# Kernel tuning notes

Measured on AMD Instinct MI355X. Metric: run time of the kernel, lower is better.

Reference implementation:

```python
import math
import jax, jax.numpy as jnp
import numpy as np

N = 2048          # batch size
D = 256           # embedding_dim
MEM = 16384       # memory_size
ANOMALY_WEIGHT = 1.0
TEMP = 0.1
MOMENTUM = 0.01
NCLS = 2          # binary phishing labels -> max(labels.max()+1, 2) == 2


def setup_inputs() -> dict:
    key = jax.random.key(0)
    ks = jax.random.split(key, 10)
    s = 1.0 / math.sqrt(D)  # nn.Linear default init range
    return {
        'z': jax.random.normal(ks[0], (N, D), jnp.float32),
        'labels': jax.random.randint(ks[1], (N,), 0, NCLS),
        'memory': jax.random.normal(ks[2], (MEM, D), jnp.float32),
        'memory_weights': jax.random.uniform(ks[3], (MEM,), jnp.float32),
        'running_mean': jnp.zeros((D,), jnp.float32),
        'running_cov': jnp.eye(D, dtype=jnp.float32),
        'Wq': jax.random.uniform(ks[4], (D, D), jnp.float32, -s, s),
        'bq': jax.random.uniform(ks[5], (D,), jnp.float32, -s, s),
        'Wk': jax.random.uniform(ks[6], (D, D), jnp.float32, -s, s),
        'bk': jax.random.uniform(ks[7], (D,), jnp.float32, -s, s),
        'Wv': jax.random.uniform(ks[8], (D, D), jnp.float32, -s, s),
        'bv': jax.random.uniform(ks[9], (D,), jnp.float32, -s, s),
    }


def reference(z, labels, memory, memory_weights, running_mean, running_cov,
              Wq, bq, Wk, bk, Wv, bv):
    # ---- update(z.detach(), labels): entire update path is detached in torch ----
    z_sg = jax.lax.stop_gradient(z)

    # _update_stats: EMA of batch mean / covariance (done before importance)
    mu = z_sg.mean(axis=0)                                  # [D]
    zc = z_sg - mu
    cov = zc.T @ zc / max(N - 1, 1)                         # [D, D]
    rm = (1.0 - MOMENTUM) * running_mean + MOMENTUM * mu
    rc = (1.0 - MOMENTUM) * running_cov + MOMENTUM * cov

    # _mahalanobis with updated running stats
    c = z_sg - rm
    cov_inv = jnp.linalg.inv(rc + 1e-6 * jnp.eye(D, dtype=rc.dtype))
    dist = jnp.sqrt(jnp.clip(jnp.einsum('nd,de,ne->n', c, cov_inv, c), 1e-8))
    a_norm = (dist - dist.min()) / (dist.max() - dist.min() + 1e-8)

    # _mi_proxy: KL(batch label dist || uniform), broadcast to all items
    counts = jnp.zeros((NCLS,), z.dtype).at[labels].add(1.0)
    p = counts / jnp.clip(counts.sum(), 1.0)
    # p / uniform == p * NCLS; clip inside log for safety (both classes present)
    kl = jnp.clip((p * jnp.log(jnp.clip(p * NCLS, 1e-8))).sum(), 0.0)
    importance = (1.0 + ANOMALY_WEIGHT * a_norm) * kl       # [N]

    # serial top-1 priority-queue eviction, in descending-importance order
    order = jnp.argsort(-importance)
    z_ord = z_sg[order]
    imp_ord = importance[order]

    def evict_step(state, inp):
        mem, w = state
        zi, imp = inp
        j = jnp.argmin(w)                   # weakest memory slot
        rep = imp > w[j]
        mem = mem.at[j].set(jnp.where(rep, zi, mem[j]))
        w = w.at[j].set(jnp.where(rep, imp, w[j]))
        return (mem, w), None

    (mem, _), _ = jax.lax.scan(evict_step, (memory, memory_weights), (z_ord, imp_ord))

    # ---- query(z): cross-attention over the (full) updated memory ----
    Q = z @ Wq.T + bq                       # [N, D]
    K = mem @ Wk.T + bk                     # [MEM, D]
    V = mem @ Wv.T + bv                     # [MEM, D]
    sc = (Q @ K.T) / math.sqrt(D)           # [N, MEM]
    attn = jax.nn.softmax(sc / TEMP, axis=-1)
    return z + 0.5 * (attn @ V)
```

## Files before the change

kernel.cpp:

```cpp
#include <hip/hip_runtime.h>
#include <math.h>

#define NB   2048
#define DE   256
#define MEMN 16384
#define CAND_CAP 256
#define FSPL 16
#define FKPS 1024
#define FIT  32

typedef __attribute__((ext_vector_type(8)))  short  short8;
typedef __attribute__((ext_vector_type(16))) float  float16;
typedef __attribute__((ext_vector_type(4)))  unsigned uint4v;
typedef __attribute__((ext_vector_type(2)))  unsigned uint2v;

static const size_t OFF_QB   = 0;
static const size_t OFF_KB   = 262144;
static const size_t OFF_VTB  = 2359296;
static const size_t OFF_LP   = 4456448;
static const size_t OFF_OPB  = 4521984;
static const size_t SO_A    = 0;
static const size_t SO_X    = 65536;
static const size_t SO_MUP  = 131072;
static const size_t SO_DIST = 147456;

__device__ inline unsigned short f2bf(float f) {
  unsigned u = __float_as_uint(f);
  unsigned r = (u + 0x7fffu + ((u >> 16) & 1u)) >> 16;
  return (unsigned short)r;
}
__device__ inline float bf2f(unsigned short s) {
  return __uint_as_float((unsigned)s << 16);
}

__device__ inline unsigned cvtpk_bf16(float lo, float hi) {
  unsigned r;
  asm("v_cvt_pk_bf16_f32 %0, %1, %2" : "=v"(r) : "v"(lo), "v"(hi));
  return r;
}

__device__ inline void halfswap(unsigned& lo, unsigned& hi, int h) {
#if __has_builtin(__builtin_amdgcn_permlane32_swap)
  (void)h;
  uint2v r = __builtin_amdgcn_permlane32_swap(lo, hi, false, false);
  lo = r.x; hi = r.y;
#else
  unsigned a = (unsigned)__shfl_xor((int)lo, 32, 64);
  unsigned b = (unsigned)__shfl_xor((int)hi, 32, 64);
  unsigned nlo = (h == 0) ? lo : b;
  unsigned nhi = (h == 0) ? a  : hi;
  lo = nlo; hi = nhi;
#endif
}

__device__ inline void bitonic_sort_u64(unsigned long long* key, int n, int tid, int nth) {
  for (int k = 2; k <= n; k <<= 1) {
    for (int j = k >> 1; j > 0; j >>= 1) {
      __syncthreads();
      for (int i = tid; i < n; i += nth) {
        int ixj = i ^ j;
        if (ixj > i) {
          unsigned long long a = key[i], b = key[ixj];
          bool up = ((i & k) == 0);
          if ((a > b) == up) { key[i] = b; key[ixj] = a; }
        }
      }
    }
  }
  __syncthreads();
}

__global__ __launch_bounds__(256) void mupart_kernel(const float* __restrict__ z,
                                                     float* __restrict__ mup,
                                                     float* __restrict__ Az) {
  int d = threadIdx.x;
  int r0 = blockIdx.x * 32;
  float4 zero4 = {0.f, 0.f, 0.f, 0.f};
  *(float4*)&Az[(size_t)blockIdx.x * 1024 + threadIdx.x * 4] = zero4;
  float s = 0.f;
  for (int r = 0; r < 32; ++r) s += z[(size_t)(r0 + r) * DE + d];
  mup[blockIdx.x * DE + d] = s;
}

__global__ __launch_bounds__(256) void covpart_kernel(const float* __restrict__ z,
                                                      float* __restrict__ A) {
  __shared__ float As[16][68];
  __shared__ float Bs[16][68];
  int tid = threadIdx.x, tx = tid & 15, ty = tid >> 4;
  int i0 = blockIdx.x * 64, j0 = blockIdx.y * 64;
  int nbase = blockIdx.z * 128;
  float acc[4][4] = {};
  for (int nt = 0; nt < 8; ++nt) {
    int n0 = nbase + nt * 16;
    for (int e = tid; e < 1024; e += 256) {
      int c = e & 63, nn = e >> 6;
      As[nn][c] = z[(size_t)(n0 + nn) * DE + i0 + c];
      Bs[nn][c] = z[(size_t)(n0 + nn) * DE + j0 + c];
    }
    __syncthreads();
#pragma unroll
    for (int nn = 0; nn < 16; ++nn) {
      float4 a4 = *(const float4*)&As[nn][ty * 4];
      float4 b4 = *(const float4*)&Bs[nn][tx * 4];
      acc[0][0] += a4.x*b4.x; acc[0][1] += a4.x*b4.y; acc[0][2] += a4.x*b4.z; acc[0][3] += a4.x*b4.w;
      acc[1][0] += a4.y*b4.x; acc[1][1] += a4.y*b4.y; acc[1][2] += a4.y*b4.z; acc[1][3] += a4.y*b4.w;
      acc[2][0] += a4.z*b4.x; acc[2][1] += a4.z*b4.y; acc[2][2] += a4.z*b4.z; acc[2][3] += a4.z*b4.w;
      acc[3][0] += a4.w*b4.x; acc[3][1] += a4.w*b4.y; acc[3][2] += a4.w*b4.z; acc[3][3] += a4.w*b4.w;
    }
    __syncthreads();
  }
  for (int r = 0; r < 4; ++r) {
    int i = i0 + ty * 4 + r;
    for (int c = 0; c < 4; ++c) {
      int j = j0 + tx * 4 + c;
      atomicAdd(&A[(size_t)i * DE + j], acc[r][c]);
    }
  }
}

__global__ __launch_bounds__(256) void gemmx_kernel(const float* __restrict__ ZtZ,
                                                    const float* __restrict__ rcov,
                                                    const float* __restrict__ mup,
                                                    float* __restrict__ X) {
  __shared__ float Ea[16][17];
  __shared__ float Eb[16][17];
  __shared__ float mus[256];
  int t = threadIdx.x, tx = t & 15, ty = t >> 4;
  int i0 = blockIdx.x * 16, j0 = blockIdx.y * 16;
  {
    float s = 0.f;
    for (int b = 0; b < 64; ++b) s += mup[b * DE + t];
    mus[t] = s;
  }
  __syncthreads();
  const float c1 = 0.01f / (float)(NB - 1);
  const float invN = 1.0f / (float)NB;
  float acc = 0.f;
  for (int k0 = 0; k0 < 256; k0 += 16) {
    int c = k0 + tx;
    {
      int r = i0 + ty;
      float base = 0.99f * rcov[(size_t)r * DE + c] +
                   c1 * (ZtZ[(size_t)r * DE + c] - mus[r] * mus[c] * invN);
      float e = -base;
      if (r == c) e += 1.0f - 1e-6f;
      Ea[ty][tx] = e;
    }
    {
      int r = j0 + ty;
      float base = 0.99f * rcov[(size_t)r * DE + c] +
                   c1 * (ZtZ[(size_t)r * DE + c] - mus[r] * mus[c] * invN);
      float e = -base;
      if (r == c) e += 1.0f - 1e-6f;
      Eb[ty][tx] = e;
    }
    __syncthreads();
#pragma unroll
    for (int k = 0; k < 16; ++k) acc += Ea[ty][k] * Eb[tx][k];
    __syncthreads();
  }
  int r = i0 + ty, c = j0 + tx;
  float base = 0.99f * rcov[(size_t)r * DE + c] +
               c1 * (ZtZ[(size_t)r * DE + c] - mus[r] * mus[c] * invN);
  float e = -base;
  if (r == c) e += 1.0f - 1e-6f;
  X[(size_t)r * DE + c] = acc + e + ((r == c) ? 1.0f : 0.0f);
}

__global__ __launch_bounds__(256) void dist_kernel(const float* __restrict__ z,
                                                   const float* __restrict__ rmean,
                                                   const float* __restrict__ mup,
                                                   const float* __restrict__ X,
                                                   float* __restrict__ dist) {
  __shared__ float cc[4][256];
  __shared__ float4 red[256];
  int n0 = blockIdx.x * 4, i = threadIdx.x;
  float s = 0.f;
  for (int b = 0; b < 64; ++b) s += mup[b * DE + i];
  float rmi = 0.99f * rmean[i] + 0.01f * s * (1.0f / (float)NB);
#pragma unroll
  for (int r = 0; r < 4; ++r) cc[r][i] = z[(size_t)(n0 + r) * DE + i] - rmi;
  __syncthreads();
  float y0 = 0.f, y1 = 0.f, y2 = 0.f, y3 = 0.f;
#pragma unroll 8
  for (int j = 0; j < DE; ++j) {
    float x = X[(size_t)j * DE + i];
    y0 += x * cc[0][j]; y1 += x * cc[1][j]; y2 += x * cc[2][j]; y3 += x * cc[3][j];
  }
  float4 v;
  v.x = y0 * cc[0][i]; v.y = y1 * cc[1][i]; v.z = y2 * cc[2][i]; v.w = y3 * cc[3][i];
  red[i] = v;
  __syncthreads();
  for (int sH = 128; sH > 0; sH >>= 1) {
    if (i < sH) {
      float4 a = red[i], b = red[i + sH];
      a.x += b.x; a.y += b.y; a.z += b.z; a.w += b.w;
      red[i] = a;
    }
    __syncthreads();
  }
  if (i < 4) {
    float4 tt = red[0];
    float d = (i == 0) ? tt.x : (i == 1) ? tt.y : (i == 2) ? tt.z : tt.w;
    dist[n0 + i] = sqrtf(fmaxf(d, 1e-8f));
  }
}

__global__ __launch_bounds__(1024) void update_kernel(const float* __restrict__ dist,
                                                      const int* __restrict__ labels,
                                                      const float* __restrict__ weights,
                                                      const float* __restrict__ z,
                                                      float* __restrict__ memory) {
  __shared__ unsigned long long ikeys[NB];
  __shared__ unsigned long long ck[CAND_CAP];
  __shared__ unsigned long long mred[1024];
  __shared__ int slots[CAND_CAP], srcs[CAND_CAP];
  __shared__ float smin[1024], smax[1024];
  __shared__ int scnt[1024];
  __shared__ float s_kl, s_dmin, s_inv;
  __shared__ int s_ccnt, s_m, s_stop;
  int t = threadIdx.x;

  float mn = 1e30f, mx = -1e30f; int c1 = 0;
  for (int n = t; n < NB; n += 1024) {
    float d = dist[n];
    mn = fminf(mn, d); mx = fmaxf(mx, d);
    c1 += labels[n];
  }
  smin[t] = mn; smax[t] = mx; scnt[t] = c1;
  __syncthreads();
  for (int s = 512; s > 0; s >>= 1) {
    if (t < s) {
      smin[t] = fminf(smin[t], smin[t + s]);
      smax[t] = fmaxf(smax[t], smax[t + s]);
      scnt[t] += scnt[t + s];
    }
    __syncthreads();
  }
  if (t == 0) {
    float p1 = (float)scnt[0] / (float)NB;
    float p0 = (float)(NB - scnt[0]) / (float)NB;
    float kl = p0 * logf(fmaxf(2.f * p0, 1e-8f)) + p1 * logf(fmaxf(2.f * p1, 1e-8f));
    s_kl = fmaxf(kl, 0.f);
    s_dmin = smin[0];
    s_inv = 1.0f / (smax[0] - smin[0] + 1e-8f);
    s_ccnt = 0; s_m = 0; s_stop = 0;
  }
  __syncthreads();
  float kl = s_kl;

  for (int n = t; n < NB; n += 1024) {
    float imp = (1.0f + (dist[n] - s_dmin) * s_inv) * kl;
    ikeys[n] = ((unsigned long long)(unsigned)(~__float_as_uint(imp)) << 32) | (unsigned)n;
  }
  float thresh = 2.f * kl;
  for (int j = t; j < MEMN; j += 1024) {
    float wv = weights[j];
    if (wv < thresh) {
      int p = atomicAdd(&s_ccnt, 1);
      if (p < CAND_CAP) ck[p] = ((unsigned long long)__float_as_uint(wv) << 32) | (unsigned)j;
    }
  }
  __syncthreads();
  int C = s_ccnt; if (C > CAND_CAP) C = CAND_CAP;
  for (int i = t; i < CAND_CAP; i += 1024)
    if (i >= C) ck[i] = 0xFFFFFFFFFFFFFFFFULL;
  bitonic_sort_u64(ck, CAND_CAP, t, 1024);

  float prevv = 0.f;
  for (int i = 0; i < C; ++i) {
    unsigned long long mymin = ikeys[t] < ikeys[t + 1024] ? ikeys[t] : ikeys[t + 1024];
    mred[t] = mymin;
    __syncthreads();
    for (int s = 512; s > 0; s >>= 1) {
      if (t < s) { if (mred[t + s] < mred[t]) mred[t] = mred[t + s]; }
      __syncthreads();
    }
    if (t == 0) {
      unsigned long long best = mred[0];
      float im = __uint_as_float(~(unsigned)(best >> 32));
      float wv = __uint_as_float((unsigned)(ck[i] >> 32));
      bool ok = (im > wv) && (i == 0 || prevv >= wv);
      if (ok) {
        slots[s_m] = (int)(ck[i] & 0xffffffffULL);
        srcs[s_m]  = (int)(best & 0xffffffffULL);
        s_m++;
        prevv = im;
        ikeys[(int)(best & 0xffffffffULL)] = ~0ULL;
      } else {
        s_stop = 1;
      }
    }
    __syncthreads();
    if (s_stop) break;
  }
  int m = s_m;
  for (int e = t; e < m * DE; e += 1024) {
    int i = e >> 8, d = e & 255;
    memory[(size_t)slots[i] * DE + d] = z[(size_t)srcs[i] * DE + d];
  }
}

__global__ __launch_bounds__(256, 1) void qkv_kernel(
    const float* __restrict__ z, const float* __restrict__ memory,
    const float* __restrict__ Wq, const float* __restrict__ bq,
    const float* __restrict__ Wk, const float* __restrict__ bk,
    const float* __restrict__ Wv, const float* __restrict__ bv,
    unsigned short* __restrict__ Qbf, unsigned short* __restrict__ Kbf,
    unsigned short* __restrict__ Vtb) {
  __shared__ unsigned short Bsh[64 * 264];
  int flat = blockIdx.x;
  const float *Af, *Bf, *bias;
  unsigned short* C;
  int bias_row, vtile, gx, gy, ldC;
  if (flat < 64) {
    gx = flat & 15; gy = flat >> 4;
    Af = z; Bf = Wq; bias = bq; bias_row = 0; vtile = 0; C = Qbf; ldC = DE;
  } else if (flat < 576) {
    int f = flat - 64; gx = f & 127; gy = f >> 7;
    Af = memory; Bf = Wk; bias = bk; bias_row = 0; vtile = 0; C = Kbf; ldC = DE;
  } else {
    int f = flat - 576; gx = f & 1; gy = f >> 1;
    Af = Wv; Bf = memory; bias = bv; bias_row = 1; vtile = 1; C = Vtb; ldC = 0;
  }

  int tid = threadIdx.x;
  int w = tid >> 6, lane = tid & 63;
  int m = lane & 31, h = lane >> 5;
  int arow = gx * 128 + w * 32 + m;
  int n0 = gy * 64;

  short8 af[16];
#pragma unroll
  for (int kc = 0; kc < 16; ++kc) {
    const float* src = &Af[(size_t)arow * DE + kc * 16 + h * 8];
    float4 f0 = *(const float4*)&src[0];
    float4 f1 = *(const float4*)&src[4];
    short8 v;
    v[0] = (short)f2bf(f0.x); v[1] = (short)f2bf(f0.y);
    v[2] = (short)f2bf(f0.z); v[3] = (short)f2bf(f0.w);
    v[4] = (short)f2bf(f1.x); v[5] = (short)f2bf(f1.y);
    v[6] = (short)f2bf(f1.z); v[7] = (short)f2bf(f1.w);
    af[kc] = v;
  }
  {
    int r = tid >> 2, q = tid & 3;
    const float* src = &Bf[(size_t)(n0 + r) * DE + q * 64];
    unsigned short* dst = &Bsh[r * 264 + q * 64];
#pragma unroll
    for (int j = 0; j < 8; ++j) {
      float4 f0 = *(const float4*)&src[j * 8];
      float4 f1 = *(const float4*)&src[j * 8 + 4];
      short8 v;
      v[0] = (short)f2bf(f0.x); v[1] = (short)f2bf(f0.y);
      v[2] = (short)f2bf(f0.z); v[3] = (short)f2bf(f0.w);
      v[4] = (short)f2bf(f1.x); v[5] = (short)f2bf(f1.y);
      v[6] = (short)f2bf(f1.z); v[7] = (short)f2bf(f1.w);
      *(short8*)&dst[j * 8] = v;
    }
  }
  __syncthreads();

  float16 a0 = {}, a1 = {};
#pragma unroll
  for (int kc = 0; kc < 16; ++kc) {
    short8 b0 = *(const short8*)&Bsh[(0 * 32 + m) * 264 + kc * 16 + h * 8];
    short8 b1 = *(const short8*)&Bsh[(1 * 32 + m) * 264 + kc * 16 + h * 8];
    a0 = __builtin_amdgcn_mfma_f32_32x32x16_bf16(af[kc], b0, a0, 0, 0, 0);
    a1 = __builtin_amdgcn_mfma_f32_32x32x16_bf16(af[kc], b1, a1, 0, 0, 0);
  }
#pragma unroll
  for (int r = 0; r < 16; ++r) {
    int rr = (r & 3) + 8 * (r >> 2) + 4 * h;
    int orow = gx * 128 + w * 32 + rr;
    int oc0 = n0 + m, oc1 = n0 + 32 + m;
    float bb0 = bias_row ? bias[orow] : bias[oc0];
    float bb1 = bias_row ? bias[orow] : bias[oc1];
    if (!vtile) {
      C[(size_t)orow * ldC + oc0] = f2bf(a0[r] + bb0);
      C[(size_t)orow * ldC + oc1] = f2bf(a1[r] + bb1);
    } else {
      C[(size_t)(oc0 >> 5) * 8192 + (size_t)orow * 32 + (oc0 & 31)] = f2bf(a0[r] + bb0);
      C[(size_t)(oc1 >> 5) * 8192 + (size_t)orow * 32 + (oc1 & 31)] = f2bf(a1[r] + bb1);
    }
  }
}

__global__ __launch_bounds__(256, 2) void flash_kernel(
    const unsigned short* __restrict__ Qb, const unsigned short* __restrict__ Kb,
    const unsigned short* __restrict__ Vtb, unsigned short* __restrict__ Opb,
    float* __restrict__ Lp) {
  __shared__ unsigned short Ks[32 * 264];
  __shared__ unsigned short Vs[128 * 40];

  int tid = threadIdx.x;
  int w = tid >> 6, lane = tid & 63;
  int m = lane & 31, h = lane >> 5;
  int sp = blockIdx.x, qg = blockIdx.y, dh = blockIdx.z;
  int myrow = qg * 128 + w * 32 + m;

  short8 qf[16];
#pragma unroll
  for (int kc = 0; kc < 16; ++kc)
    qf[kc] = *(const short8*)&Qb[(size_t)myrow * DE + kc * 16 + h * 8];

  float16 O[4] = {};
  float lacc = 0.f;

  short8 kreg[4], vreg[2];
  {
    int kb = sp * FKPS;
#pragma unroll
    for (int i = 0; i < 4; ++i) {
      int c = i * 256 + tid, kr = c >> 5, kc = c & 31;
      kreg[i] = *(const short8*)&Kb[(size_t)(kb + kr) * DE + kc * 8];
    }
    const unsigned short* vg = &Vtb[(size_t)(kb >> 5) * 8192 + (size_t)dh * 4096];
#pragma unroll
    for (int i = 0; i < 2; ++i) {
      int c = i * 256 + tid;
      vreg[i] = *(const short8*)&vg[c * 8];
    }
  }

  for (int it = 0; it < FIT; ++it) {
    __syncthreads();
#pragma unroll
    for (int i = 0; i < 4; ++i) {
      int c = i * 256 + tid, kr = c >> 5, kc = c & 31;
      *(short8*)&Ks[kr * 264 + kc * 8] = kreg[i];
    }
#pragma unroll
    for (int i = 0; i < 2; ++i) {
      int c = i * 256 + tid, dr = c >> 2, dc = c & 3;
      *(short8*)&Vs[dr * 40 + dc * 8] = vreg[i];
    }
    if (it + 1 < FIT) {
      int kb = sp * FKPS + (it + 1) * 32;
#pragma unroll
      for (int i = 0; i < 4; ++i) {
        int c = i * 256 + tid, kr = c >> 5, kc = c & 31;
        kreg[i] = *(const short8*)&Kb[(size_t)(kb + kr) * DE + kc * 8];
      }
      const unsigned short* vg = &Vtb[(size_t)(kb >> 5) * 8192 + (size_t)dh * 4096];
#pragma unroll
      for (int i = 0; i < 2; ++i) {
        int c = i * 256 + tid;
        vreg[i] = *(const short8*)&vg[c * 8];
      }
    }
    __syncthreads();

    float16 s0 = {}, s1 = {};
    __builtin_amdgcn_s_setprio(1);
#pragma unroll
    for (int kc = 0; kc < 16; kc += 2) {
      short8 b0 = *(const short8*)&Ks[m * 264 + kc * 16 + h * 8];
      short8 b1 = *(const short8*)&Ks[m * 264 + (kc + 1) * 16 + h * 8];
      s0 = __builtin_amdgcn_mfma_f32_32x32x16_bf16(b0, qf[kc], s0, 0, 0, 0);
      s1 = __builtin_amdgcn_mfma_f32_32x32x16_bf16(b1, qf[kc + 1], s1, 0, 0, 0);
    }
    __builtin_amdgcn_s_setprio(0);

    float p[16];
#pragma unroll
    for (int r = 0; r < 16; ++r)
      p[r] = exp2f(fmaf(s0[r] + s1[r], 0.90168440f, -16.0f));

    lacc += ((p[0] + p[1]) + (p[2] + p[3])) + ((p[4] + p[5]) + (p[6] + p[7])) +
            ((p[8] + p[9]) + (p[10] + p[11])) + ((p[12] + p[13]) + (p[14] + p[15]));

    unsigned c0 = cvtpk_bf16(p[0],  p[1]);
    unsigned c1 = cvtpk_bf16(p[2],  p[3]);
    unsigned c2 = cvtpk_bf16(p[4],  p[5]);
    unsigned c3 = cvtpk_bf16(p[6],  p[7]);
    unsigned c4 = cvtpk_bf16(p[8],  p[9]);
    unsigned c5 = cvtpk_bf16(p[10], p[11]);
    unsigned c6 = cvtpk_bf16(p[12], p[13]);
    unsigned c7 = cvtpk_bf16(p[14], p[15]);
    halfswap(c0, c2, h);
    halfswap(c1, c3, h);
    halfswap(c4, c6, h);
    halfswap(c5, c7, h);
    uint4v w0v = {c0, c1, c2, c3};
    uint4v w1v = {c4, c5, c6, c7};
    short8 pa0 = __builtin_bit_cast(short8, w0v);
    short8 pa1 = __builtin_bit_cast(short8, w1v);

    __builtin_amdgcn_s_setprio(1);
#pragma unroll
    for (int ct = 0; ct < 4; ++ct) {
      short8 vb0 = *(const short8*)&Vs[(ct * 32 + m) * 40 + h * 8];
      short8 vb1 = *(const short8*)&Vs[(ct * 32 + m) * 40 + 16 + h * 8];
      O[ct] = __builtin_amdgcn_mfma_f32_32x32x16_bf16(pa0, vb0, O[ct], 0, 0, 0);
      O[ct] = __builtin_amdgcn_mfma_f32_32x32x16_bf16(pa1, vb1, O[ct], 0, 0, 0);
    }
    __builtin_amdgcn_s_setprio(0);
  }

  size_t ob = ((size_t)sp * NB + qg * 128 + w * 32) * DE + dh * 128;
#pragma unroll
  for (int ct = 0; ct < 4; ++ct)
#pragma unroll
    for (int r = 0; r < 16; ++r) {
      int rr = (r & 3) + 8 * (r >> 2) + 4 * h;
      Opb[ob + (size_t)rr * DE + ct * 32 + m] = f2bf(O[ct][r]);
    }
  float ltot = lacc + __shfl_xor(lacc, 32, 64);
  if (dh == 0 && h == 0)
    Lp[sp * NB + qg * 128 + w * 32 + m] = ltot;
}

__global__ __launch_bounds__(256) void combine_kernel(const float* __restrict__ z,
                                                      const unsigned short* __restrict__ Opb,
                                                      const float* __restrict__ Lp,
                                                      float* __restrict__ out) {
  int n = blockIdx.x, c = threadIdx.x;
  float num = 0.f, den = 0.f;
#pragma unroll
  for (int s = 0; s < FSPL; ++s) {
    den += Lp[s * NB + n];
    num += bf2f(Opb[((size_t)s * NB + n) * DE + c]);
  }
  size_t base = (size_t)n * DE + c;
  out[base] = z[base] + 0.5f * num / den;
}

extern "C" void kernel_launch(void* const* d_in, const int* in_sizes, int n_in,
                              void* d_out, int out_size, void* d_ws, size_t ws_size,
                              hipStream_t stream) {
  (void)in_sizes; (void)n_in; (void)out_size; (void)ws_size;
  const float* z       = (const float*)d_in[0];
  const int*   labels  = (const int*)d_in[1];
  float*       memory  = (float*)d_in[2];
  const float* weights = (const float*)d_in[3];
  const float* rmean   = (const float*)d_in[4];
  const float* rcov    = (const float*)d_in[5];
  const float* Wq      = (const float*)d_in[6];
  const float* bq      = (const float*)d_in[7];
  const float* Wk      = (const float*)d_in[8];
  const float* bk      = (const float*)d_in[9];
  const float* Wv      = (const float*)d_in[10];
  const float* bv      = (const float*)d_in[11];
  float* out = (float*)d_out;
  float* ws  = (float*)d_ws;

  unsigned short* Qbf = (unsigned short*)(ws + OFF_QB);
  unsigned short* Kbf = (unsigned short*)(ws + OFF_KB);
  unsigned short* Vtb = (unsigned short*)(ws + OFF_VTB);
  float* Lp           = ws + OFF_LP;
  unsigned short* Opb = (unsigned short*)(ws + OFF_OPB);
  float* SB    = ws + OFF_OPB;
  float* A     = SB + SO_A;
  float* X     = SB + SO_X;
  float* mup   = SB + SO_MUP;
  float* dist  = SB + SO_DIST;

  mupart_kernel<<<64, 256, 0, stream>>>(z, mup, A);
  covpart_kernel<<<dim3(4, 4, 16), 256, 0, stream>>>(z, A);
  gemmx_kernel<<<dim3(16, 16), 256, 0, stream>>>(A, rcov, mup, X);
  dist_kernel<<<NB / 4, 256, 0, stream>>>(z, rmean, mup, X, dist);
  update_kernel<<<1, 1024, 0, stream>>>(dist, labels, weights, z, memory);
  qkv_kernel<<<1088, 256, 0, stream>>>(z, memory, Wq, bq, Wk, bk, Wv, bv, Qbf, Kbf, Vtb);
  flash_kernel<<<dim3(FSPL, NB / 128, 2), 256, 0, stream>>>(Qbf, Kbf, Vtb, Opb, Lp);
  combine_kernel<<<NB, 256, 0, stream>>>(z, Opb, Lp, out);
}
```

Baseline: 260.0 us.

## Use warp-shuffle reductions in update kernel and double flash key tile size

The update kernel's block-wide shared-memory tree reductions become wave-level shuffle reductions. The serial eviction loop now keeps per-wave minima and recomputes only the wave whose entry was consumed, which removes about ten barriers per eviction step. The flash kernel processes 64 keys per iteration instead of 32, halving the number of barrier-separated load/store stages. The cost is doubled LDS and register use for K/V staging, which may lower occupancy.

```diff
diff --git a/kernel.cpp b/kernel.cpp
--- a/kernel.cpp
+++ b/kernel.cpp
@@ -7,7 +7,7 @@
 #define CAND_CAP 256
 #define FSPL 16
 #define FKPS 1024
-#define FIT  32
+#define FIT  16
 
 typedef __attribute__((ext_vector_type(8)))  short  short8;
 typedef __attribute__((ext_vector_type(16))) float  float16;
@@ -213,13 +213,14 @@
                                                       float* __restrict__ memory) {
   __shared__ unsigned long long ikeys[NB];
   __shared__ unsigned long long ck[CAND_CAP];
-  __shared__ unsigned long long mred[1024];
+  __shared__ unsigned long long gmin[16];
   __shared__ int slots[CAND_CAP], srcs[CAND_CAP];
-  __shared__ float smin[1024], smax[1024];
-  __shared__ int scnt[1024];
+  __shared__ float smin[16], smax[16];
+  __shared__ int scnt[16];
   __shared__ float s_kl, s_dmin, s_inv;
-  __shared__ int s_ccnt, s_m, s_stop;
+  __shared__ int s_ccnt, s_m, s_stop, s_bg;
   int t = threadIdx.x;
+  int wid = t >> 6, lane = t & 63;
 
   float mn = 1e30f, mx = -1e30f; int c1 = 0;
   for (int n = t; n < NB; n += 1024) {
@@ -227,24 +228,24 @@
     mn = fminf(mn, d); mx = fmaxf(mx, d);
     c1 += labels[n];
   }
-  smin[t] = mn; smax[t] = mx; scnt[t] = c1;
-  __syncthreads();
-  for (int s = 512; s > 0; s >>= 1) {
-    if (t < s) {
-      smin[t] = fminf(smin[t], smin[t + s]);
-      smax[t] = fmaxf(smax[t], smax[t + s]);
-      scnt[t] += scnt[t + s];
-    }
-    __syncthreads();
-  }
+#pragma unroll
+  for (int o = 32; o > 0; o >>= 1) {
+    mn = fminf(mn, __shfl_xor(mn, o, 64));
+    mx = fmaxf(mx, __shfl_xor(mx, o, 64));
+    c1 += __shfl_xor(c1, o, 64);
+  }
+  if (lane == 0) { smin[wid] = mn; smax[wid] = mx; scnt[wid] = c1; }
+  if (t == 0) { s_ccnt = 0; s_m = 0; s_stop = 0; }
+  __syncthreads();
   if (t == 0) {
-    float p1 = (float)scnt[0] / (float)NB;
-    float p0 = (float)(NB - scnt[0]) / (float)NB;
+    float a = 1e30f, b = -1e30f; int cc = 0;
+    for (int i = 0; i < 16; ++i) { a = fminf(a, smin[i]); b = fmaxf(b, smax[i]); cc += scnt[i]; }
+    float p1 = (float)cc / (float)NB;
+    float p0 = (float)(NB - cc) / (float)NB;
     float kl = p0 * logf(fmaxf(2.f * p0, 1e-8f)) + p1 * logf(fmaxf(2.f * p1, 1e-8f));
     s_kl = fmaxf(kl, 0.f);
-    s_dmin = smin[0];
-    s_inv = 1.0f / (smax[0] - smin[0] + 1e-8f);
-    s_ccnt = 0; s_m = 0; s_stop = 0;
+    s_dmin = a;
+    s_inv = 1.0f / (b - a + 1e-8f);
   }
   __syncthreads();
   float kl = s_kl;
@@ -267,32 +268,53 @@
     if (i >= C) ck[i] = 0xFFFFFFFFFFFFFFFFULL;
   bitonic_sort_u64(ck, CAND_CAP, t, 1024);
 
+  {
+    unsigned long long a = ikeys[wid * 128 + lane];
+    unsigned long long b = ikeys[wid * 128 + 64 + lane];
+    unsigned long long mm = a < b ? a : b;
+#pragma unroll
+    for (int o = 32; o > 0; o >>= 1) {
+      unsigned long long ot = (unsigned long long)__shfl_xor((long long)mm, o, 64);
+      if (ot < mm) mm = ot;
+    }
+    if (lane == 0) gmin[wid] = mm;
+  }
+  __syncthreads();
+
   float prevv = 0.f;
   for (int i = 0; i < C; ++i) {
-    unsigned long long mymin = ikeys[t] < ikeys[t + 1024] ? ikeys[t] : ikeys[t + 1024];
-    mred[t] = mymin;
-    __syncthreads();
-    for (int s = 512; s > 0; s >>= 1) {
-      if (t < s) { if (mred[t + s] < mred[t]) mred[t] = mred[t + s]; }
-      __syncthreads();
-    }
     if (t == 0) {
-      unsigned long long best = mred[0];
+      unsigned long long best = 0xFFFFFFFFFFFFFFFFULL;
+      for (int g = 0; g < 16; ++g) if (gmin[g] < best) best = gmin[g];
       float im = __uint_as_float(~(unsigned)(best >> 32));
       float wv = __uint_as_float((unsigned)(ck[i] >> 32));
       bool ok = (im > wv) && (i == 0 || prevv >= wv);
       if (ok) {
+        int idx = (int)(best & 0xffffffffULL);
         slots[s_m] = (int)(ck[i] & 0xffffffffULL);
-        srcs[s_m]  = (int)(best & 0xffffffffULL);
+        srcs[s_m]  = idx;
         s_m++;
         prevv = im;
-        ikeys[(int)(best & 0xffffffffULL)] = ~0ULL;
+        ikeys[idx] = 0xFFFFFFFFFFFFFFFFULL;
+        s_bg = idx >> 7;
       } else {
-        s_stop = 1;
+        s_stop = 1; s_bg = -1;
       }
     }
     __syncthreads();
     if (s_stop) break;
+    if (wid == s_bg) {
+      unsigned long long a = ikeys[wid * 128 + lane];
+      unsigned long long b = ikeys[wid * 128 + 64 + lane];
+      unsigned long long mm = a < b ? a : b;
+#pragma unroll
+      for (int o = 32; o > 0; o >>= 1) {
+        unsigned long long ot = (unsigned long long)__shfl_xor((long long)mm, o, 64);
+        if (ot < mm) mm = ot;
+      }
+      if (lane == 0) gmin[wid] = mm;
+    }
+    __syncthreads();
   }
   int m = s_m;
   for (int e = t; e < m * DE; e += 1024) {
@@ -390,8 +412,8 @@
     const unsigned short* __restrict__ Qb, const unsigned short* __restrict__ Kb,
     const unsigned short* __restrict__ Vtb, unsigned short* __restrict__ Opb,
     float* __restrict__ Lp) {
-  __shared__ unsigned short Ks[32 * 264];
-  __shared__ unsigned short Vs[128 * 40];
+  __shared__ unsigned short Ks[64 * 264];
+  __shared__ unsigned short Vs[256 * 40];
 
   int tid = threadIdx.x;
   int w = tid >> 6, lane = tid & 63;
@@ -407,96 +429,96 @@
   float16 O[4] = {};
   float lacc = 0.f;
 
-  short8 kreg[4], vreg[2];
-  {
-    int kb = sp * FKPS;
-#pragma unroll
-    for (int i = 0; i < 4; ++i) {
-      int c = i * 256 + tid, kr = c >> 5, kc = c & 31;
-      kreg[i] = *(const short8*)&Kb[(size_t)(kb + kr) * DE + kc * 8];
-    }
-    const unsigned short* vg = &Vtb[(size_t)(kb >> 5) * 8192 + (size_t)dh * 4096];
-#pragma unroll
-    for (int i = 0; i < 2; ++i) {
-      int c = i * 256 + tid;
-      vreg[i] = *(const short8*)&vg[c * 8];
-    }
-  }
+  short8 kreg[8], vreg[4];
+#define LOAD_TILES(kb_)                                                              \
+  {                                                                                  \
+    int kb = (kb_);                                                                  \
+    _Pragma("unroll")                                                                \
+    for (int i = 0; i < 8; ++i) {                                                    \
+      int c = i * 256 + tid, kr = c >> 5, kcol = c & 31;                             \
+      kreg[i] = *(const short8*)&Kb[(size_t)(kb + kr) * DE + kcol * 8];              \
+    }                                                                                \
+    const unsigned short* vg = &Vtb[(size_t)((kb) >> 5) * 8192 + (size_t)dh * 4096]; \
+    _Pragma("unroll")                                                                \
+    for (int i = 0; i < 4; ++i) {                                                    \
+      int c = i * 256 + tid;                                                         \
+      int sub = c >> 9, cc = c & 511;                                                \
+      vreg[i] = *(const short8*)&vg[(size_t)sub * 8192 + cc * 8];                    \
+    }                                                                                \
+  }
+#define STORE_TILES()                                                                \
+  {                                                                                  \
+    _Pragma("unroll")                                                                \
+    for (int i = 0; i < 8; ++i) {                                                    \
+      int c = i * 256 + tid, kr = c >> 5, kcol = c & 31;                             \
+      *(short8*)&Ks[kr * 264 + kcol * 8] = kreg[i];                                  \
+    }                                                                                \
+    _Pragma("unroll")                                                                \
+    for (int i = 0; i < 4; ++i) {                                                    \
+      int c = i * 256 + tid, dr = c >> 2, dc = c & 3;                                \
+      *(short8*)&Vs[dr * 40 + dc * 8] = vreg[i];                                     \
+    }                                                                                \
+  }
+
+  LOAD_TILES(sp * FKPS);
 
   for (int it = 0; it < FIT; ++it) {
     __syncthreads();
-#pragma unroll
-    for (int i = 0; i < 4; ++i) {
-      int c = i * 256 + tid, kr = c >> 5, kc = c & 31;
-      *(short8*)&Ks[kr * 264 + kc * 8] = kreg[i];
-    }
-#pragma unroll
-    for (int i = 0; i < 2; ++i) {
-      int c = i * 256 + tid, dr = c >> 2, dc = c & 3;
-      *(short8*)&Vs[dr * 40 + dc * 8] = vreg[i];
-    }
-    if (it + 1 < FIT) {
-      int kb = sp * FKPS + (it + 1) * 32;
-#pragma unroll
-      for (int i = 0; i < 4; ++i) {
-        int c = i * 256 + tid, kr = c >> 5, kc = c & 31;
-        kreg[i] = *(const short8*)&Kb[(size_t)(kb + kr) * DE + kc * 8];
+    STORE_TILES();
+    if (it + 1 < FIT) LOAD_TILES(sp * FKPS + (it + 1) * 64);
+    __syncthreads();
+
+#pragma unroll
+    for (int sub = 0; sub < 2; ++sub) {
+      float16 s0 = {}, s1 = {};
+      __builtin_amdgcn_s_setprio(1);
+#pragma unroll
+      for (int kc = 0; kc < 16; kc += 2) {
+        short8 b0 = *(const short8*)&Ks[(sub * 32 + m) * 264 + kc * 16 + h * 8];
+        short8 b1 = *(const short8*)&Ks[(sub * 32 + m) * 264 + (kc + 1) * 16 + h * 8];
+        s0 = __builtin_amdgcn_mfma_f32_32x32x16_bf16(b0, qf[kc], s0, 0, 0, 0);
+        s1 = __builtin_amdgcn_mfma_f32_32x32x16_bf16(b1, qf[kc + 1], s1, 0, 0, 0);
       }
-      const unsigned short* vg = &Vtb[(size_t)(kb >> 5) * 8192 + (size_t)dh * 4096];
-#pragma unroll
-      for (int i = 0; i < 2; ++i) {
-        int c = i * 256 + tid;
-        vreg[i] = *(const short8*)&vg[c * 8];
+      __builtin_amdgcn_s_setprio(0);
+
+      float p[16];
+#pragma unroll
+      for (int r = 0; r < 16; ++r)
+        p[r] = exp2f(fmaf(s0[r] + s1[r], 0.90168440f, -16.0f));
+
+      lacc += ((p[0] + p[1]) + (p[2] + p[3])) + ((p[4] + p[5]) + (p[6] + p[7])) +
+              ((p[8] + p[9]) + (p[10] + p[11])) + ((p[12] + p[13]) + (p[14] + p[15]));
+
+      unsigned c0 = cvtpk_bf16(p[0],  p[1]);
+      unsigned c1 = cvtpk_bf16(p[2],  p[3]);
+      unsigned c2 = cvtpk_bf16(p[4],  p[5]);
+      unsigned c3 = cvtpk_bf16(p[6],  p[7]);
+      unsigned c4 = cvtpk_bf16(p[8],  p[9]);
+      unsigned c5 = cvtpk_bf16(p[10], p[11]);
+      unsigned c6 = cvtpk_bf16(p[12], p[13]);
+      unsigned c7 = cvtpk_bf16(p[14], p[15]);
+      halfswap(c0, c2, h);
+      halfswap(c1, c3, h);
+      halfswap(c4, c6, h);
+      halfswap(c5, c7, h);
+      uint4v w0v = {c0, c1, c2, c3};
+      uint4v w1v = {c4, c5, c6, c7};
+      short8 pa0 = __builtin_bit_cast(short8, w0v);
+      short8 pa1 = __builtin_bit_cast(short8, w1v);
+
+      __builtin_amdgcn_s_setprio(1);
+#pragma unroll
+      for (int ct = 0; ct < 4; ++ct) {
+        short8 vb0 = *(const short8*)&Vs[(sub * 128 + ct * 32 + m) * 40 + h * 8];
+        short8 vb1 = *(const short8*)&Vs[(sub * 128 + ct * 32 + m) * 40 + 16 + h * 8];
+        O[ct] = __builtin_amdgcn_mfma_f32_32x32x16_bf16(pa0, vb0, O[ct], 0, 0, 0);
+        O[ct] = __builtin_amdgcn_mfma_f32_32x32x16_bf16(pa1, vb1, O[ct], 0, 0, 0);
       }
-    }
-    __syncthreads();
-
-    float16 s0 = {}, s1 = {};
-    __builtin_amdgcn_s_setprio(1);
-#pragma unroll
-    for (int kc = 0; kc < 16; kc += 2) {
-      short8 b0 = *(const short8*)&Ks[m * 264 + kc * 16 + h * 8];
-      short8 b1 = *(const short8*)&Ks[m * 264 + (kc + 1) * 16 + h * 8];
-      s0 = __builtin_amdgcn_mfma_f32_32x32x16_bf16(b0, qf[kc], s0, 0, 0, 0);
-      s1 = __builtin_amdgcn_mfma_f32_32x32x16_bf16(b1, qf[kc + 1], s1, 0, 0, 0);
-    }
-    __builtin_amdgcn_s_setprio(0);
-
-    float p[16];
-#pragma unroll
-    for (int r = 0; r < 16; ++r)
-      p[r] = exp2f(fmaf(s0[r] + s1[r], 0.90168440f, -16.0f));
-
-    lacc += ((p[0] + p[1]) + (p[2] + p[3])) + ((p[4] + p[5]) + (p[6] + p[7])) +
-            ((p[8] + p[9]) + (p[10] + p[11])) + ((p[12] + p[13]) + (p[14] + p[15]));
-
-    unsigned c0 = cvtpk_bf16(p[0],  p[1]);
-    unsigned c1 = cvtpk_bf16(p[2],  p[3]);
-    unsigned c2 = cvtpk_bf16(p[4],  p[5]);
-    unsigned c3 = cvtpk_bf16(p[6],  p[7]);
-    unsigned c4 = cvtpk_bf16(p[8],  p[9]);
-    unsigned c5 = cvtpk_bf16(p[10], p[11]);
-    unsigned c6 = cvtpk_bf16(p[12], p[13]);
-    unsigned c7 = cvtpk_bf16(p[14], p[15]);
-    halfswap(c0, c2, h);
-    halfswap(c1, c3, h);
-    halfswap(c4, c6, h);
-    halfswap(c5, c7, h);
-    uint4v w0v = {c0, c1, c2, c3};
-    uint4v w1v = {c4, c5, c6, c7};
-    short8 pa0 = __builtin_bit_cast(short8, w0v);
-    short8 pa1 = __builtin_bit_cast(short8, w1v);
-
-    __builtin_amdgcn_s_setprio(1);
-#pragma unroll
-    for (int ct = 0; ct < 4; ++ct) {
-      short8 vb0 = *(const short8*)&Vs[(ct * 32 + m) * 40 + h * 8];
-      short8 vb1 = *(const short8*)&Vs[(ct * 32 + m) * 40 + 16 + h * 8];
-      O[ct] = __builtin_amdgcn_mfma_f32_32x32x16_bf16(pa0, vb0, O[ct], 0, 0, 0);
-      O[ct] = __builtin_amdgcn_mfma_f32_32x32x16_bf16(pa1, vb1, O[ct], 0, 0, 0);
-    }
-    __builtin_amdgcn_s_setprio(0);
-  }
+      __builtin_amdgcn_s_setprio(0);
+    }
+  }
+#undef LOAD_TILES
+#undef STORE_TILES
 
   size_t ob = ((size_t)sp * NB + qg * 128 + w * 32) * DE + dh * 128;
 #pragma unroll
```

New measurement: 258.9 us. No clear change (-0.4%).
